# Performance work log

Hardware: AMD Instinct MI355X
Metric: run time of the kernel (lower is better)

Reference implementation:

```python
import jax, jax.numpy as jnp
import numpy as np

N = 50000      # nodes
E = 800000     # edges
D = 128        # input feature dim
H = 8          # heads
C = 16         # out_channels per head (H*C == D, concat output width == D)
SLOPE = 0.2    # PyG GATConv leaky_relu negative slope


def gat_layer(x, src, dst, W, a_src, a_dst, b):
    # linear transform, shared for src/dst (PyG GATConv with int in_channels)
    h = (x @ W).reshape(N, H, C)                      # [N,H,C]
    alpha_src = jnp.einsum('nhc,hc->nh', h, a_src)    # [N,H]
    alpha_dst = jnp.einsum('nhc,hc->nh', h, a_dst)    # [N,H]
    e = jax.nn.leaky_relu(alpha_src[src] + alpha_dst[dst], SLOPE)  # [E,H]
    # segment softmax over edges grouped by destination node
    emax = jax.ops.segment_max(e, dst, num_segments=N)            # [N,H]
    emax = jnp.where(jnp.isfinite(emax), emax, 0.0)               # nodes with no in-edges
    ex = jnp.exp(e - emax[dst])                                   # [E,H]
    denom = jax.ops.segment_sum(ex, dst, num_segments=N)          # [N,H]
    alpha = ex / (denom[dst] + 1e-16)                             # [E,H]
    # weighted scatter-aggregate of source messages
    out = jax.ops.segment_sum(h[src] * alpha[:, :, None], dst, num_segments=N)  # [N,H,C]
    return out.reshape(N, H * C) + b, alpha


def setup_inputs() -> dict:
    key = jax.random.key(0)
    ks = jax.random.split(key, 10)
    s = 1.0 / np.sqrt(D)
    return {
        'x': jax.random.normal(ks[0], (N, D), dtype=jnp.float32),
        'W1': jax.random.normal(ks[1], (D, H * C), dtype=jnp.float32) * s,
        'a_src1': jax.random.normal(ks[2], (H, C), dtype=jnp.float32) * s,
        'a_dst1': jax.random.normal(ks[3], (H, C), dtype=jnp.float32) * s,
        'b1': jnp.zeros((H * C,), dtype=jnp.float32),
        'W2': jax.random.normal(ks[4], (H * C, H * C), dtype=jnp.float32) * s,
        'a_src2': jax.random.normal(ks[5], (H, C), dtype=jnp.float32) * s,
        'a_dst2': jax.random.normal(ks[6], (H, C), dtype=jnp.float32) * s,
        'b2': jnp.zeros((H * C,), dtype=jnp.float32),
        'edge_index': jax.random.randint(ks[7], (2, E), 0, N, dtype=jnp.int64),
    }


def reference(x, W1, a_src1, a_dst1, b1, W2, a_src2, a_dst2, b2, edge_index):
    src, dst = edge_index[0], edge_index[1]
    x1, alpha1 = gat_layer(x, src, dst, W1, a_src1, a_dst1, b1)
    x2, alpha2 = gat_layer(x1, src, dst, W2, a_src2, a_dst2, b2)
    # matches torch forward: (x, attention_weights per layer)
    return x2, alpha1, alpha2
```

## Files before the change

kernel.cpp:

```cpp
#include <hip/hip_runtime.h>
#include <hip/hip_fp16.h>

#define NN 50000
#define NE 800000
#define SLOPE 0.2f
#define NEG_INF (-1e30f)
#define SCAN_B 196
#define ECAP 64

typedef _Float16 half8 __attribute__((ext_vector_type(8)));
typedef float f32x4 __attribute__((ext_vector_type(4)));
typedef unsigned int u32x4 __attribute__((ext_vector_type(4)));

__device__ __forceinline__ float lrelu(float v) { return v >= 0.f ? v : SLOPE * v; }

__global__ __launch_bounds__(256) void prep_all(
    const float* __restrict__ W1, const float* __restrict__ as1, const float* __restrict__ ad1,
    __half* __restrict__ WT1,
    const float* __restrict__ W2, const float* __restrict__ as2, const float* __restrict__ ad2,
    __half* __restrict__ WT2,
    int* __restrict__ counts)
{
    const int t0 = blockIdx.x * 256 + threadIdx.x;
    const int stride = gridDim.x * 256;
    for (int i = t0; i < NN; i += stride) counts[i] = 0;
    #pragma unroll
    for (int layer = 0; layer < 2; ++layer) {
        const float* W = layer ? W2 : W1;
        const float* as_ = layer ? as2 : as1;
        const float* ad_ = layer ? ad2 : ad1;
        __half* WT = layer ? WT2 : WT1;
        for (int idx = t0; idx < 1024; idx += stride) {
            const int k = idx >> 3, h = idx & 7;
            float s1 = 0.f, s2 = 0.f;
            #pragma unroll
            for (int c = 0; c < 16; ++c) {
                const float w = W[k * 128 + h * 16 + c];
                s1 += w * as_[h * 16 + c];
                s2 += w * ad_[h * 16 + c];
            }
            WT[(size_t)(128 + h) * 128 + k] = (__half)s1;
            WT[(size_t)(136 + h) * 128 + k] = (__half)s2;
        }
        for (int idx = t0; idx < 16384; idx += stride) {
            const int k = idx >> 7, c = idx & 127;
            WT[(size_t)c * 128 + k] = (__half)W[idx];
        }
    }
}

template<bool F32IN>
__global__ __launch_bounds__(256) void mfma_gemm(
    const void* __restrict__ Xin, const __half* __restrict__ WT,
    __half* __restrict__ H16, float* __restrict__ asrc, float* __restrict__ adst)
{
    const int t = threadIdx.x;
    const int w = t >> 6;
    const int lane = t & 63;
    const int r16 = lane & 15;
    const int g = lane >> 4;
    const int rowStrip = blockIdx.x * 64 + w * 16;
    const int rowm = min(rowStrip + r16, NN - 1);

    half8 afr[4];
    if constexpr (F32IN) {
        const float* xr = (const float*)Xin + (size_t)rowm * 128;
        #pragma unroll
        for (int ks = 0; ks < 4; ++ks) {
            const int k0 = ks * 32 + 8 * g;
            const float4 p = *(const float4*)&xr[k0];
            const float4 q = *(const float4*)&xr[k0 + 4];
            half8 a;
            a[0] = (_Float16)p.x; a[1] = (_Float16)p.y; a[2] = (_Float16)p.z; a[3] = (_Float16)p.w;
            a[4] = (_Float16)q.x; a[5] = (_Float16)q.y; a[6] = (_Float16)q.z; a[7] = (_Float16)q.w;
            afr[ks] = a;
        }
    } else {
        const __half* xr = (const __half*)Xin + (size_t)rowm * 128;
        #pragma unroll
        for (int ks = 0; ks < 4; ++ks) {
            afr[ks] = *(const half8*)&xr[ks * 32 + 8 * g];
        }
    }

    for (int ct = 0; ct < 9; ++ct) {
        f32x4 acc = {0.f, 0.f, 0.f, 0.f};
        const __half* wrow = WT + (size_t)(ct * 16 + r16) * 128 + 8 * g;
        #pragma unroll
        for (int ks = 0; ks < 4; ++ks) {
            const half8 b = *(const half8*)&wrow[ks * 32];
            acc = __builtin_amdgcn_mfma_f32_16x16x32_f16(afr[ks], b, acc, 0, 0, 0);
        }
        if (ct < 8) {
            #pragma unroll
            for (int rr = 0; rr < 4; ++rr) {
                const int r = rowStrip + 4 * g + rr;
                if (r < NN) H16[(size_t)r * 128 + ct * 16 + r16] = (__half)acc[rr];
            }
        } else {
            #pragma unroll
            for (int rr = 0; rr < 4; ++rr) {
                const int r = rowStrip + 4 * g + rr;
                if (r < NN) {
                    if (r16 < 8) asrc[(size_t)r * 8 + r16] = acc[rr];
                    else         adst[(size_t)r * 8 + (r16 - 8)] = acc[rr];
                }
            }
        }
    }
}

__global__ __launch_bounds__(256) void hist_rank(
    const int* __restrict__ dst, int* __restrict__ counts, int* __restrict__ rank) {
    int e = blockIdx.x * 256 + threadIdx.x;
    if (e >= NE) return;
    int d = dst[e];
    if ((unsigned)d >= NN) d = 0;
    rank[e] = atomicAdd(&counts[d], 1);
}

__global__ __launch_bounds__(256) void block_sum(const int* __restrict__ counts,
                                                 int* __restrict__ bsum) {
    __shared__ int red[256];
    int t = threadIdx.x, i = blockIdx.x * 256 + t;
    red[t] = (i < NN) ? counts[i] : 0;
    __syncthreads();
    for (int s = 128; s > 0; s >>= 1) {
        if (t < s) red[t] += red[t + s];
        __syncthreads();
    }
    if (t == 0) bsum[blockIdx.x] = red[0];
}

__global__ __launch_bounds__(256) void scan_bsum(const int* __restrict__ bsum,
                                                 int* __restrict__ boff) {
    __shared__ int sh[256];
    int t = threadIdx.x;
    int v = (t < SCAN_B) ? bsum[t] : 0;
    sh[t] = v;
    __syncthreads();
    for (int d = 1; d < 256; d <<= 1) {
        int u = (t >= d) ? sh[t - d] : 0;
        __syncthreads();
        sh[t] += u;
        __syncthreads();
    }
    if (t < SCAN_B) boff[t] = sh[t] - v;
}

__global__ __launch_bounds__(256) void scan_final(
    const int* __restrict__ counts, const int* __restrict__ boff,
    int* __restrict__ off)
{
    __shared__ int sh[256];
    int t = threadIdx.x, i = blockIdx.x * 256 + t;
    int v = (i < NN) ? counts[i] : 0;
    sh[t] = v;
    __syncthreads();
    for (int d = 1; d < 256; d <<= 1) {
        int u = (t >= d) ? sh[t - d] : 0;
        __syncthreads();
        sh[t] += u;
        __syncthreads();
    }
    if (i < NN) {
        int o = boff[blockIdx.x] + sh[t] - v;
        off[i] = o;
        if (i == NN - 1) off[NN] = o + v;
    }
}

__global__ __launch_bounds__(256) void place_csr(
    const int* __restrict__ src, const int* __restrict__ dst,
    const int* __restrict__ rank, const int* __restrict__ off,
    int2* __restrict__ csrES) {
    int e = blockIdx.x * 256 + threadIdx.x;
    if (e >= NE) return;
    int s = src[e], d = dst[e];
    if ((unsigned)s >= NN) s = 0;
    if ((unsigned)d >= NN) d = 0;
    int pos = off[d] + rank[e];
    unsigned long long v = ((unsigned long long)(unsigned)s << 32) | (unsigned)e;
    __builtin_nontemporal_store(v, (unsigned long long*)&csrES[pos]);
}

template<typename OT, bool NTOUT>
__global__ __launch_bounds__(256) void node_fused(
    const int* __restrict__ off, const int2* __restrict__ csrES,
    const float* __restrict__ asrc, const float* __restrict__ adst,
    const __half* __restrict__ H16, const float* __restrict__ bias,
    float* __restrict__ alpha, OT* __restrict__ out)
{
    __shared__ float ecache[4][ECAP * 8];
    __shared__ int2  scache[4][ECAP];
    const int w = threadIdx.x >> 6;
    int wid = (blockIdx.x * 256 + threadIdx.x) >> 6;
    if (wid >= NN) return;
    const int lane = threadIdx.x & 63;
    const int n = wid;
    const int p0 = off[n], p1 = off[n + 1];
    const int deg = p1 - p0;
    const int h = lane & 7;
    const int el = lane >> 3;
    const float ad = adst[n * 8 + h];

    float m = NEG_INF, l = 0.f;
    for (int base = 0; base < deg; base += 8) {
        int i = base + el;
        if (i < deg) {
            int2 es = csrES[p0 + i];
            float v = lrelu(asrc[es.y * 8 + h] + ad);
            if (i < ECAP) {
                ecache[w][i * 8 + h] = v;
                if (h == 0) scache[w][i] = es;
            }
            float nm = fmaxf(m, v);
            l = l * __expf(m - nm) + __expf(v - nm);
            m = nm;
        }
    }
    #pragma unroll
    for (int msk = 8; msk <= 32; msk <<= 1) {
        float m2 = __shfl_xor(m, msk);
        float l2 = __shfl_xor(l, msk);
        float nm = fmaxf(m, m2);
        l = l * __expf(m - nm) + l2 * __expf(m2 - nm);
        m = nm;
    }
    const float inv = 1.f / (l + 1e-16f);

    const int q  = lane >> 4;
    const int ql = lane & 15;
    const int hq = ql >> 1;
    float4 accA = make_float4(0.f, 0.f, 0.f, 0.f);
    float4 accB = make_float4(0.f, 0.f, 0.f, 0.f);
    for (int base = 0; base < deg; base += 8) {
        int i = base + el;
        float a = 0.f;
        int s = 0;
        if (i < deg) {
            int e;
            float v;
            if (i < ECAP) {
                int2 es = scache[w][i];
                e = es.x; s = es.y;
                v = ecache[w][i * 8 + h];
            } else {
                int2 es = csrES[p0 + i];
                e = es.x; s = es.y;
                v = lrelu(asrc[s * 8 + h] + ad);
            }
            a = __expf(v - m) * inv;
            __builtin_nontemporal_store(a, &alpha[(size_t)e * 8 + h]);
        }
        const int cnt = min(8, deg - base);
        for (int kb = 0; kb < cnt; kb += 4) {
            const int kw = kb + q;
            const int kc = min(kw, cnt - 1);
            float ak = __shfl(a, kc * 8 + hq);
            int   sk = __shfl(s, kc * 8);
            const float am = (kw < cnt) ? ak : 0.f;
            float4 raw = *(const float4*)&H16[(size_t)sk * 128 + ql * 8];
            const __half2* ph = (const __half2*)&raw;
            const float2 f0 = __half22float2(ph[0]);
            const float2 f1 = __half22float2(ph[1]);
            const float2 f2 = __half22float2(ph[2]);
            const float2 f3 = __half22float2(ph[3]);
            accA.x = fmaf(f0.x, am, accA.x);
            accA.y = fmaf(f0.y, am, accA.y);
            accA.z = fmaf(f1.x, am, accA.z);
            accA.w = fmaf(f1.y, am, accA.w);
            accB.x = fmaf(f2.x, am, accB.x);
            accB.y = fmaf(f2.y, am, accB.y);
            accB.z = fmaf(f3.x, am, accB.z);
            accB.w = fmaf(f3.y, am, accB.w);
        }
    }
    accA.x += __shfl_xor(accA.x, 16); accA.x += __shfl_xor(accA.x, 32);
    accA.y += __shfl_xor(accA.y, 16); accA.y += __shfl_xor(accA.y, 32);
    accA.z += __shfl_xor(accA.z, 16); accA.z += __shfl_xor(accA.z, 32);
    accA.w += __shfl_xor(accA.w, 16); accA.w += __shfl_xor(accA.w, 32);
    accB.x += __shfl_xor(accB.x, 16); accB.x += __shfl_xor(accB.x, 32);
    accB.y += __shfl_xor(accB.y, 16); accB.y += __shfl_xor(accB.y, 32);
    accB.z += __shfl_xor(accB.z, 16); accB.z += __shfl_xor(accB.z, 32);
    accB.w += __shfl_xor(accB.w, 16); accB.w += __shfl_xor(accB.w, 32);
    if (q == 0) {
        const float4 bva = *(const float4*)&bias[ql * 8];
        const float4 bvb = *(const float4*)&bias[ql * 8 + 4];
        const float o0 = accA.x + bva.x, o1 = accA.y + bva.y;
        const float o2 = accA.z + bva.z, o3 = accA.w + bva.w;
        const float o4 = accB.x + bvb.x, o5 = accB.y + bvb.y;
        const float o6 = accB.z + bvb.z, o7 = accB.w + bvb.w;
        if constexpr (sizeof(OT) == 4) {
            if constexpr (NTOUT) {
                f32x4 oa = {o0, o1, o2, o3}, ob = {o4, o5, o6, o7};
                __builtin_nontemporal_store(oa, (f32x4*)&out[(size_t)n * 128 + ql * 8]);
                __builtin_nontemporal_store(ob, (f32x4*)&out[(size_t)n * 128 + ql * 8 + 4]);
            } else {
                float4 oa = {o0, o1, o2, o3}, ob = {o4, o5, o6, o7};
                *(float4*)&out[(size_t)n * 128 + ql * 8]     = oa;
                *(float4*)&out[(size_t)n * 128 + ql * 8 + 4] = ob;
            }
        } else {
            __half2 p0h = __floats2half2_rn(o0, o1);
            __half2 p1h = __floats2half2_rn(o2, o3);
            __half2 p2h = __floats2half2_rn(o4, o5);
            __half2 p3h = __floats2half2_rn(o6, o7);
            u32x4 pk = {*(unsigned*)&p0h, *(unsigned*)&p1h, *(unsigned*)&p2h, *(unsigned*)&p3h};
            if constexpr (NTOUT) {
                __builtin_nontemporal_store(pk, (u32x4*)&out[(size_t)n * 128 + ql * 8]);
            } else {
                *(u32x4*)&out[(size_t)n * 128 + ql * 8] = pk;
            }
        }
    }
}

extern "C" void kernel_launch(void* const* d_in, const int* in_sizes, int n_in,
                              void* d_out, int out_size, void* d_ws, size_t ws_size,
                              hipStream_t stream)
{
    const float* x   = (const float*)d_in[0];
    const float* W1  = (const float*)d_in[1];
    const float* as1 = (const float*)d_in[2];
    const float* ad1 = (const float*)d_in[3];
    const float* b1  = (const float*)d_in[4];
    const float* W2  = (const float*)d_in[5];
    const float* as2 = (const float*)d_in[6];
    const float* ad2 = (const float*)d_in[7];
    const float* b2  = (const float*)d_in[8];
    const int*   ei  = (const int*)d_in[9];
    const int* srcp = ei;
    const int* dstp = ei + NE;

    float* outx   = (float*)d_out;
    float* alpha1 = outx + (size_t)NN * 128;
    float* alpha2 = alpha1 + (size_t)NE * 8;

    __half* h16 = (__half*)d_ws;
    __half* x1h = h16 + (size_t)NN * 128;
    __half* wt1 = x1h + (size_t)NN * 128;
    __half* wt2 = wt1 + (size_t)144 * 128;
    float* asrc = (float*)(wt2 + (size_t)144 * 128);
    float* adst = asrc + (size_t)NN * 8;
    int* counts = (int*)(adst + (size_t)NN * 8);
    int* off    = counts + NN;
    int* rank   = off + NN + 1;
    int2* csrES = (int2*)(rank + NE);
    int* bsum   = (int*)(csrES + NE);
    int* boff   = bsum + SCAN_B;

    int gemmGrid = (NN + 63) / 64;
    int nodeGrid = (NN + 3) / 4;
    int edgeGrid = (NE + 255) / 256;

    prep_all<<<SCAN_B, 256, 0, stream>>>(W1, as1, ad1, wt1, W2, as2, ad2, wt2, counts);
    hist_rank<<<edgeGrid, 256, 0, stream>>>(dstp, counts, rank);
    block_sum<<<SCAN_B, 256, 0, stream>>>(counts, bsum);
    scan_bsum<<<1, 256, 0, stream>>>(bsum, boff);
    scan_final<<<SCAN_B, 256, 0, stream>>>(counts, boff, off);
    place_csr<<<edgeGrid, 256, 0, stream>>>(srcp, dstp, rank, off, csrES);

    mfma_gemm<true><<<gemmGrid, 256, 0, stream>>>(x, wt1, h16, asrc, adst);
    node_fused<__half, false><<<nodeGrid, 256, 0, stream>>>(off, csrES, asrc, adst, h16, b1, alpha1, x1h);

    mfma_gemm<false><<<gemmGrid, 256, 0, stream>>>(x1h, wt2, h16, asrc, adst);
    node_fused<float, true><<<nodeGrid, 256, 0, stream>>>(off, csrES, asrc, adst, h16, b2, alpha2, outx);
}
```

Measured before the change: 233.1 us.

## Replace per-node max pass with global alpha_src max bound for single-pass softmax

The GEMM now computes a global per-head maximum of alpha_src through atomicMax on order-preserving unsigned keys. Each node uses lrelu(globalmax + adst) as a softmax shift bound, so the separate online max/sum pass is dropped. Exponentials, the denominator and the weighted aggregation are fused into one edge loop, and normalisation is applied afterwards. This saves one pass over edges and the gathers of asrc per node. The cost is 8 atomics per GEMM block and a risk of underflow when the global bound sits far above a node's true maximum.

Result: slower. 289.1 us (+24.1%).

```diff
diff --git a/kernel.cpp b/kernel.cpp
--- a/kernel.cpp
+++ b/kernel.cpp
@@ -4,7 +4,6 @@
 #define NN 50000
 #define NE 800000
 #define SLOPE 0.2f
-#define NEG_INF (-1e30f)
 #define SCAN_B 196
 #define ECAP 64
 
@@ -13,17 +12,25 @@
 typedef unsigned int u32x4 __attribute__((ext_vector_type(4)));
 
 __device__ __forceinline__ float lrelu(float v) { return v >= 0.f ? v : SLOPE * v; }
+__device__ __forceinline__ unsigned int f2u(float f) {
+    unsigned int b = __float_as_uint(f);
+    return (b & 0x80000000u) ? ~b : (b | 0x80000000u);
+}
+__device__ __forceinline__ float u2f(unsigned int u) {
+    return __uint_as_float((u & 0x80000000u) ? (u & 0x7fffffffu) : ~u);
+}
 
 __global__ __launch_bounds__(256) void prep_all(
     const float* __restrict__ W1, const float* __restrict__ as1, const float* __restrict__ ad1,
     __half* __restrict__ WT1,
     const float* __restrict__ W2, const float* __restrict__ as2, const float* __restrict__ ad2,
     __half* __restrict__ WT2,
-    int* __restrict__ counts)
+    int* __restrict__ counts, unsigned int* __restrict__ gm1, unsigned int* __restrict__ gm2)
 {
     const int t0 = blockIdx.x * 256 + threadIdx.x;
     const int stride = gridDim.x * 256;
     for (int i = t0; i < NN; i += stride) counts[i] = 0;
+    if (t0 < 8) { gm1[t0] = f2u(-1e30f); gm2[t0] = f2u(-1e30f); }
     #pragma unroll
     for (int layer = 0; layer < 2; ++layer) {
         const float* W = layer ? W2 : W1;
@@ -52,7 +59,8 @@
 template<bool F32IN>
 __global__ __launch_bounds__(256) void mfma_gemm(
     const void* __restrict__ Xin, const __half* __restrict__ WT,
-    __half* __restrict__ H16, float* __restrict__ asrc, float* __restrict__ adst)
+    __half* __restrict__ H16, float* __restrict__ asrc, float* __restrict__ adst,
+    unsigned int* __restrict__ gmaxE)
 {
     const int t = threadIdx.x;
     const int w = t >> 6;
@@ -98,6 +106,7 @@
                 if (r < NN) H16[(size_t)r * 128 + ct * 16 + r16] = (__half)acc[rr];
             }
         } else {
+            float lmax = fmaxf(fmaxf(acc[0], acc[1]), fmaxf(acc[2], acc[3]));
             #pragma unroll
             for (int rr = 0; rr < 4; ++rr) {
                 const int r = rowStrip + 4 * g + rr;
@@ -106,6 +115,9 @@
                     else         adst[(size_t)r * 8 + (r16 - 8)] = acc[rr];
                 }
             }
+            lmax = fmaxf(lmax, __shfl_xor(lmax, 16));
+            lmax = fmaxf(lmax, __shfl_xor(lmax, 32));
+            if (g == 0 && r16 < 8) atomicMax(&gmaxE[r16], f2u(lmax));
         }
     }
 }
@@ -188,10 +200,11 @@
 __global__ __launch_bounds__(256) void node_fused(
     const int* __restrict__ off, const int2* __restrict__ csrES,
     const float* __restrict__ asrc, const float* __restrict__ adst,
+    const unsigned int* __restrict__ gmaxE,
     const __half* __restrict__ H16, const float* __restrict__ bias,
     float* __restrict__ alpha, OT* __restrict__ out)
 {
-    __shared__ float ecache[4][ECAP * 8];
+    __shared__ float pcache[4][ECAP * 8];
     __shared__ int2  scache[4][ECAP];
     const int w = threadIdx.x >> 6;
     int wid = (blockIdx.x * 256 + threadIdx.x) >> 6;
@@ -203,79 +216,72 @@
     const int h = lane & 7;
     const int el = lane >> 3;
     const float ad = adst[n * 8 + h];
-
-    float m = NEG_INF, l = 0.f;
-    for (int base = 0; base < deg; base += 8) {
-        int i = base + el;
-        if (i < deg) {
-            int2 es = csrES[p0 + i];
-            float v = lrelu(asrc[es.y * 8 + h] + ad);
-            if (i < ECAP) {
-                ecache[w][i * 8 + h] = v;
-                if (h == 0) scache[w][i] = es;
-            }
-            float nm = fmaxf(m, v);
-            l = l * __expf(m - nm) + __expf(v - nm);
-            m = nm;
-        }
-    }
-    #pragma unroll
-    for (int msk = 8; msk <= 32; msk <<= 1) {
-        float m2 = __shfl_xor(m, msk);
-        float l2 = __shfl_xor(l, msk);
-        float nm = fmaxf(m, m2);
-        l = l * __expf(m - nm) + l2 * __expf(m2 - nm);
-        m = nm;
-    }
-    const float inv = 1.f / (l + 1e-16f);
+    const float M = lrelu(u2f(gmaxE[h]) + ad);
 
     const int q  = lane >> 4;
     const int ql = lane & 15;
     const int hq = ql >> 1;
+
+    float l = 0.f;
     float4 accA = make_float4(0.f, 0.f, 0.f, 0.f);
     float4 accB = make_float4(0.f, 0.f, 0.f, 0.f);
+
     for (int base = 0; base < deg; base += 8) {
         int i = base + el;
-        float a = 0.f;
+        float p = 0.f;
         int s = 0;
         if (i < deg) {
-            int e;
-            float v;
+            int2 es = csrES[p0 + i];
+            s = es.y;
+            float v = lrelu(asrc[s * 8 + h] + ad);
+            p = __expf(v - M);
+            l += p;
             if (i < ECAP) {
-                int2 es = scache[w][i];
-                e = es.x; s = es.y;
-                v = ecache[w][i * 8 + h];
-            } else {
-                int2 es = csrES[p0 + i];
-                e = es.x; s = es.y;
-                v = lrelu(asrc[s * 8 + h] + ad);
-            }
-            a = __expf(v - m) * inv;
-            __builtin_nontemporal_store(a, &alpha[(size_t)e * 8 + h]);
+                pcache[w][i * 8 + h] = p;
+                if (h == 0) scache[w][i] = es;
+            }
         }
         const int cnt = min(8, deg - base);
         for (int kb = 0; kb < cnt; kb += 4) {
             const int kw = kb + q;
             const int kc = min(kw, cnt - 1);
-            float ak = __shfl(a, kc * 8 + hq);
+            float pk = __shfl(p, kc * 8 + hq);
             int   sk = __shfl(s, kc * 8);
-            const float am = (kw < cnt) ? ak : 0.f;
+            const float pm = (kw < cnt) ? pk : 0.f;
             float4 raw = *(const float4*)&H16[(size_t)sk * 128 + ql * 8];
             const __half2* ph = (const __half2*)&raw;
             const float2 f0 = __half22float2(ph[0]);
             const float2 f1 = __half22float2(ph[1]);
             const float2 f2 = __half22float2(ph[2]);
             const float2 f3 = __half22float2(ph[3]);
-            accA.x = fmaf(f0.x, am, accA.x);
-            accA.y = fmaf(f0.y, am, accA.y);
-            accA.z = fmaf(f1.x, am, accA.z);
-            accA.w = fmaf(f1.y, am, accA.w);
-            accB.x = fmaf(f2.x, am, accB.x);
-            accB.y = fmaf(f2.y, am, accB.y);
-            accB.z = fmaf(f3.x, am, accB.z);
-            accB.w = fmaf(f3.y, am, accB.w);
-        }
-    }
+            accA.x = fmaf(f0.x, pm, accA.x);
+            accA.y = fmaf(f0.y, pm, accA.y);
+            accA.z = fmaf(f1.x, pm, accA.z);
+            accA.w = fmaf(f1.y, pm, accA.w);
+            accB.x = fmaf(f2.x, pm, accB.x);
+            accB.y = fmaf(f2.y, pm, accB.y);
+            accB.z = fmaf(f3.x, pm, accB.z);
+            accB.w = fmaf(f3.y, pm, accB.w);
+        }
+    }
+    l += __shfl_xor(l, 8);
+    l += __shfl_xor(l, 16);
+    l += __shfl_xor(l, 32);
+    const float inv = 1.f / (l + 1e-16f);
+
+    for (int i = el; i < deg && i < ECAP; i += 8) {
+        int2 es = scache[w][i];
+        __builtin_nontemporal_store(pcache[w][i * 8 + h] * inv,
+                                    &alpha[(size_t)es.x * 8 + h]);
+    }
+    for (int i = ECAP + el; i < deg; i += 8) {
+        int2 es = csrES[p0 + i];
+        float v = lrelu(asrc[es.y * 8 + h] + ad);
+        __builtin_nontemporal_store(__expf(v - M) * inv,
+                                    &alpha[(size_t)es.x * 8 + h]);
+    }
+
+    const float invH = __shfl(inv, hq);
     accA.x += __shfl_xor(accA.x, 16); accA.x += __shfl_xor(accA.x, 32);
     accA.y += __shfl_xor(accA.y, 16); accA.y += __shfl_xor(accA.y, 32);
     accA.z += __shfl_xor(accA.z, 16); accA.z += __shfl_xor(accA.z, 32);
@@ -287,10 +293,10 @@
     if (q == 0) {
         const float4 bva = *(const float4*)&bias[ql * 8];
         const float4 bvb = *(const float4*)&bias[ql * 8 + 4];
-        const float o0 = accA.x + bva.x, o1 = accA.y + bva.y;
-        const float o2 = accA.z + bva.z, o3 = accA.w + bva.w;
-        const float o4 = accB.x + bvb.x, o5 = accB.y + bvb.y;
-        const float o6 = accB.z + bvb.z, o7 = accB.w + bvb.w;
+        const float o0 = accA.x * invH + bva.x, o1 = accA.y * invH + bva.y;
+        const float o2 = accA.z * invH + bva.z, o3 = accA.w * invH + bva.w;
+        const float o4 = accB.x * invH + bvb.x, o5 = accB.y * invH + bvb.y;
+        const float o6 = accB.z * invH + bvb.z, o7 = accB.w * invH + bvb.w;
         if constexpr (sizeof(OT) == 4) {
             if constexpr (NTOUT) {
                 f32x4 oa = {o0, o1, o2, o3}, ob = {o4, o5, o6, o7};
@@ -349,21 +355,23 @@
     int2* csrES = (int2*)(rank + NE);
     int* bsum   = (int*)(csrES + NE);
     int* boff   = bsum + SCAN_B;
+    unsigned int* gm1 = (unsigned int*)(boff + SCAN_B);
+    unsigned int* gm2 = gm1 + 8;
 
     int gemmGrid = (NN + 63) / 64;
     int nodeGrid = (NN + 3) / 4;
     int edgeGrid = (NE + 255) / 256;
 
-    prep_all<<<SCAN_B, 256, 0, stream>>>(W1, as1, ad1, wt1, W2, as2, ad2, wt2, counts);
+    prep_all<<<SCAN_B, 256, 0, stream>>>(W1, as1, ad1, wt1, W2, as2, ad2, wt2, counts, gm1, gm2);
     hist_rank<<<edgeGrid, 256, 0, stream>>>(dstp, counts, rank);
     block_sum<<<SCAN_B, 256, 0, stream>>>(counts, bsum);
     scan_bsum<<<1, 256, 0, stream>>>(bsum, boff);
     scan_final<<<SCAN_B, 256, 0, stream>>>(counts, boff, off);
     place_csr<<<edgeGrid, 256, 0, stream>>>(srcp, dstp, rank, off, csrES);
 
-    mfma_gemm<true><<<gemmGrid, 256, 0, stream>>>(x, wt1, h16, asrc, adst);
-    node_fused<__half, false><<<nodeGrid, 256, 0, stream>>>(off, csrES, asrc, adst, h16, b1, alpha1, x1h);
-
-    mfma_gemm<false><<<gemmGrid, 256, 0, stream>>>(x1h, wt2, h16, asrc, adst);
-    node_fused<float, true><<<nodeGrid, 256, 0, stream>>>(off, csrES, asrc, adst, h16, b2, alpha2, outx);
-}
+    mfma_gemm<true><<<gemmGrid, 256, 0, stream>>>(x, wt1, h16, asrc, adst, gm1);
+    node_fused<__half, false><<<nodeGrid, 256, 0, stream>>>(off, csrES, asrc, adst, gm1, h16, b1, alpha1, x1h);
+
+    mfma_gemm<false><<<gemmGrid, 256, 0, stream>>>(x1h, wt2, h16, asrc, adst, gm2);
+    node_fused<float, true><<<nodeGrid, 256, 0, stream>>>(off, csrES, asrc, adst, gm2, h16, b2, alpha2, outx);
+}
```
